# Performance work log

Measured on AMD Instinct MI355X. Metric: run time of the kernel, lower is better.

The kernel has to match this reference:

```python
import jax, jax.numpy as jnp
import numpy as np
from jax import lax


def _conv(x, w, b, stride, pad):
    y = lax.conv_general_dilated(
        x, w, window_strides=(stride, stride),
        padding=[(pad, pad), (pad, pad)],
        dimension_numbers=('NCHW', 'OIHW', 'NCHW'))
    return y + b[None, :, None, None]


def _maxpool3s2(x):
    return lax.reduce_window(x, -jnp.inf, lax.max,
                             (1, 1, 3, 3), (1, 1, 2, 2), 'VALID')


def setup_inputs() -> dict:
    key = jax.random.key(0)
    ks = jax.random.split(key, 16)
    s = 0.05  # weight scale for numerical sanity
    inp = {
        'x': jax.random.normal(ks[0], (128, 3, 224, 224), jnp.float32),
        'w1': jax.random.normal(ks[1], (64, 3, 3, 3), jnp.float32) * s,
        'b1': jnp.zeros((64,), jnp.float32),
        'w2': jax.random.normal(ks[2], (192, 64, 5, 5), jnp.float32) * s,
        'b2': jnp.zeros((192,), jnp.float32),
        'w3': jax.random.normal(ks[3], (384, 192, 3, 3), jnp.float32) * s,
        'b3': jnp.zeros((384,), jnp.float32),
        'w4': jax.random.normal(ks[4], (256, 384, 3, 3), jnp.float32) * s,
        'b4': jnp.zeros((256,), jnp.float32),
        'w5': jax.random.normal(ks[5], (256, 256, 3, 3), jnp.float32) * s,
        'b5': jnp.zeros((256,), jnp.float32),
        'fc1_w': jax.random.normal(ks[6], (4096, 9216), jnp.float32) * 0.01,
        'fc1_b': jnp.zeros((4096,), jnp.float32),
        'fc2_w': jax.random.normal(ks[7], (4096, 4096), jnp.float32) * 0.01,
        'fc2_b': jnp.zeros((4096,), jnp.float32),
        'fc3_w': jax.random.normal(ks[8], (10, 4096), jnp.float32) * 0.01,
        'fc3_b': jnp.zeros((10,), jnp.float32),
        # uniform(0.1, 0.3) per element, matching random.uniform(0.1, 0.3)
        'unif': jax.random.uniform(ks[9], (128, 10), jnp.float32, 0.1, 0.3),
        # np.random.normal(0, 1) noise
        'noise': jax.random.normal(ks[10], (128, 10), jnp.float32),
    }
    return inp


def _forward(x, w1, b1, w2, b2, w3, b3, w4, b4, w5, b5,
             fc1_w, fc1_b, fc2_w, fc2_b, fc3_w, fc3_b, unif, noise):
    # features
    h = jax.nn.relu(_conv(x, w1, b1, stride=4, pad=2))   # [B,64,57,57]
    h = _maxpool3s2(h)                                   # [B,64,28,28]
    h = jax.nn.relu(_conv(h, w2, b2, stride=1, pad=2))   # [B,192,28,28]
    h = _maxpool3s2(h)                                   # [B,192,13,13]
    h = jax.nn.relu(_conv(h, w3, b3, stride=1, pad=1))   # [B,384,13,13]
    h = jax.nn.relu(_conv(h, w4, b4, stride=1, pad=1))   # [B,256,13,13]
    h = jax.nn.relu(_conv(h, w5, b5, stride=1, pad=1))   # [B,256,13,13]
    h = _maxpool3s2(h)                                   # [B,256,6,6]
    # adaptive avgpool to (6,6) is identity at this spatial size
    h = h.reshape(h.shape[0], 256 * 6 * 6)               # [B,9216]
    # classifier (Dropout = identity in eval mode)
    h = jax.nn.relu(h @ fc1_w.T + fc1_b)                 # [B,4096]
    h = jax.nn.relu(h @ fc2_w.T + fc2_b)                 # [B,4096]
    logits = h @ fc3_w.T + fc3_b                         # [B,10]
    # post: keep argmax entry, replace others with unif*max (detached),
    # add Gaussian noise, softmax
    m = jnp.max(logits, axis=-1, keepdims=True)          # [B,1]
    idx = jnp.argmax(logits, axis=-1, keepdims=True)     # first max, like torch
    onehot = jnp.arange(logits.shape[-1])[None, :] == idx
    filled = jnp.where(onehot, logits, unif * lax.stop_gradient(m))
    return jax.nn.softmax(filled + noise, axis=-1)


def reference(x, w1, b1, w2, b2, w3, b3, w4, b4, w5, b5,
              fc1_w, fc1_b, fc2_w, fc2_b, fc3_w, fc3_b, unif, noise):
    return _forward(x, w1, b1, w2, b2, w3, b3, w4, b4, w5, b5,
                    fc1_w, fc1_b, fc2_w, fc2_b, fc3_w, fc3_b, unif, noise)
```

## Files before the change

### kernel.cpp

```cpp
#include <hip/hip_runtime.h>
#include <math.h>


typedef __attribute__((ext_vector_type(4))) float  f32x4;
typedef __attribute__((ext_vector_type(8))) short  bf16x8;

#define OFF_C1O      25690112ull
#define OFF_X2H      0ull
#define OFF_X2L      12845056ull
#define OFF_WT2H     25690112ull
#define OFF_WT2L     26304512ull
#define OFF_WT3H     26918912ull
#define OFF_WT3L     28246016ull
#define OFF_WT4H     29573120ull
#define OFF_WT4L     31342592ull
#define OFF_WT5H     33112064ull
#define OFF_WT5L     34291712ull
#define OFF_Y2H      36000000ull
#define OFF_Y2L      74535168ull
#define OFF_X3H      113100000ull
#define OFF_X3L      121406688ull
#define OFF_Y3H      36000000ull
#define OFF_Y3L      52613376ull
#define OFF_Y4H      70000000ull
#define OFF_Y4L      81075584ull
#define OFF_Y5H      93000000ull
#define OFF_Y5L      104075584ull
#define OFF_P3       0ull
#define OFF_FC1      5000000ull
#define OFF_FC2      8000000ull
#define OFF_LOG      11000000ull
#define OFF_PART     40000000ull

__device__ inline void bf16split(float v, unsigned short& h, unsigned short& l) {
  unsigned u = __builtin_bit_cast(unsigned, v);
  unsigned hb = (u + 0x7fffu + ((u >> 16) & 1u)) >> 16;
  h = (unsigned short)hb;
  float hf = __builtin_bit_cast(float, hb << 16);
  float r = v - hf;
  unsigned u2 = __builtin_bit_cast(unsigned, r);
  l = (unsigned short)((u2 + 0x7fffu + ((u2 >> 16) & 1u)) >> 16);
}
__device__ inline void bf16split_fast(float v, unsigned short& h, unsigned short& l) {
  unsigned u = __builtin_bit_cast(unsigned, v);
  h = (unsigned short)(u >> 16);
  float r = v - __builtin_bit_cast(float, u & 0xFFFF0000u);
  unsigned u2 = __builtin_bit_cast(unsigned, r);
  l = (unsigned short)((u2 + 0x7fffu + ((u2 >> 16) & 1u)) >> 16);
}
__device__ inline float bf2f(unsigned short h) {
  return __builtin_bit_cast(float, ((unsigned)h) << 16);
}

__global__ __launch_bounds__(256) void conv1_kernel(
    const float* __restrict__ x, const float* __restrict__ w,
    const float* __restrict__ bias, float* __restrict__ out) {
  const int b = blockIdx.y;
  const int s = blockIdx.x * 256 + threadIdx.x;
  if (s >= 57 * 57) return;
  const int oh = s / 57, ow = s % 57;
  float iv[27];
#pragma unroll
  for (int ci = 0; ci < 3; ++ci)
#pragma unroll
    for (int kh = 0; kh < 3; ++kh)
#pragma unroll
      for (int kw = 0; kw < 3; ++kw) {
        const int ih = oh * 4 - 2 + kh;
        const int iw = ow * 4 - 2 + kw;
        float v = 0.f;
        if (ih >= 0 && ih < 224 && iw >= 0 && iw < 224)
          v = x[(((size_t)b * 3 + ci) * 224 + ih) * 224 + iw];
        iv[ci * 9 + kh * 3 + kw] = v;
      }
  for (int co = 0; co < 64; ++co) {
    float a = bias[co];
#pragma unroll
    for (int p = 0; p < 27; ++p) a = fmaf(w[co * 27 + p], iv[p], a);
    out[((size_t)b * 64 + co) * 3249 + s] = fmaxf(a, 0.f);
  }
}

__global__ __launch_bounds__(256) void pool1cvt_kernel(
    const float* __restrict__ in, unsigned short* __restrict__ xh,
    unsigned short* __restrict__ xl) {
  const int tid = blockIdx.x * 256 + threadIdx.x;
  if (tid >= 128 * 784) return;
  const int b = tid / 784, s = tid % 784;
  const int oh = s / 28, ow = s % 28;
  const float* base = in + (size_t)b * 64 * 3249 + (size_t)(oh * 2) * 57 + ow * 2;
  for (int cg = 0; cg < 16; ++cg) {
    unsigned short h[4], l[4];
#pragma unroll
    for (int j = 0; j < 4; ++j) {
      const float* p = base + (size_t)(cg * 4 + j) * 3249;
      float m = -INFINITY;
#pragma unroll
      for (int kh = 0; kh < 3; ++kh)
#pragma unroll
        for (int kw = 0; kw < 3; ++kw) m = fmaxf(m, p[kh * 57 + kw]);
      bf16split(m, h[j], l[j]);
    }
    const size_t g = ((size_t)b * 784 + s) * 64 + cg * 4;
    *reinterpret_cast<uint2*>(xh + g) =
        make_uint2((unsigned)h[0] | ((unsigned)h[1] << 16),
                   (unsigned)h[2] | ((unsigned)h[3] << 16));
    *reinterpret_cast<uint2*>(xl + g) =
        make_uint2((unsigned)l[0] | ((unsigned)l[1] << 16),
                   (unsigned)l[2] | ((unsigned)l[3] << 16));
  }
}

__global__ void wtrans_hl_kernel(const float* __restrict__ w,
                                 unsigned short* __restrict__ wh,
                                 unsigned short* __restrict__ wl,
                                 int C_in, int P, int C_out) {
  const int ncc = C_in >> 5;
  const int total = C_out * P * C_in;
  for (int e = blockIdx.x * blockDim.x + threadIdx.x; e < total;
       e += gridDim.x * blockDim.x) {
    const int ci_in = e & 31;
    int t1 = e >> 5;
    const int fr = t1 & 15;
    int t2 = t1 >> 4;
    const int cc = t2 % ncc;
    int t3 = t2 / ncc;
    const int p = t3 % P;
    const int ct = t3 / P;
    const int co = ct * 16 + fr;
    const int ci = cc * 32 + ci_in;
    const float v = w[((size_t)co * C_in + ci) * P + p];
    unsigned short h, l;
    bf16split(v, h, l);
    wh[e] = h; wl[e] = l;
  }
}

__global__ __launch_bounds__(256, 2) void conv2_mfma_kernel(
    const unsigned short* __restrict__ xh, const unsigned short* __restrict__ xl,
    const unsigned short* __restrict__ wh, const unsigned short* __restrict__ wl,
    const float* __restrict__ bias,
    unsigned short* __restrict__ yh, unsigned short* __restrict__ yl) {
  __shared__ unsigned short xt_h[352 * 40];
  __shared__ unsigned short xt_l[352 * 40];
  const int t = threadIdx.x;
  const int lane = t & 63, wv = t >> 6;
  const int b = blockIdx.x;
  const int rg = blockIdx.y;
  const int cg = blockIdx.z;
  const int fr = lane & 15, fq = lane >> 4;
  const int k0 = fq * 8;
  const int frag = fr * 32 + k0;

  int bofs[4];
  bool act[4];
#pragma unroll
  for (int ti = 0; ti < 4; ++ti) {
    const int tile = ti * 4 + wv;
    act[ti] = (tile <= 12);
    int n = tile * 16 + fr;
    if (tile > 12 || n > 195) n = 195;
    const int r = n / 28, c = n % 28;
    bofs[ti] = (r * 32 + c) * 40 + k0;
  }

  f32x4 acc[4][4];
#pragma unroll
  for (int i = 0; i < 4; ++i)
#pragma unroll
    for (int j = 0; j < 4; ++j) acc[i][j] = (f32x4){0.f, 0.f, 0.f, 0.f};

  for (int cc = 0; cc < 2; ++cc) {
    __syncthreads();
    for (int e = t; e < 1408; e += 256) {
      const int sp = e >> 2, kg = e & 3;
      const int hr = sp >> 5, hc = sp & 31;
      const int ih = rg * 7 + hr - 2, ic = hc - 2;
      uint4 vh = make_uint4(0, 0, 0, 0), vl = make_uint4(0, 0, 0, 0);
      if (ih >= 0 && ih < 28 && ic >= 0 && ic < 28) {
        const size_t g = ((size_t)b * 784 + ih * 28 + ic) * 64 + cc * 32 + kg * 8;
        vh = *reinterpret_cast<const uint4*>(xh + g);
        vl = *reinterpret_cast<const uint4*>(xl + g);
      }
      *reinterpret_cast<uint4*>(xt_h + sp * 40 + kg * 8) = vh;
      *reinterpret_cast<uint4*>(xt_l + sp * 40 + kg * 8) = vl;
    }
    __syncthreads();
#pragma unroll 5
    for (int p = 0; p < 25; ++p) {
      bf16x8 a_h[4], a_l[4];
#pragma unroll
      for (int cot = 0; cot < 4; ++cot) {
        const size_t wg = ((((size_t)(cg * 4 + cot) * 25 + p) * 2 + cc) << 9) + frag;
        a_h[cot] = __builtin_bit_cast(bf16x8, *reinterpret_cast<const uint4*>(wh + wg));
        a_l[cot] = __builtin_bit_cast(bf16x8, *reinterpret_cast<const uint4*>(wl + wg));
      }
      const int kh = p / 5, kw = p % 5;
      const int poff = (kh * 32 + kw) * 40;
      bf16x8 bh[4], bl[4];
#pragma unroll
      for (int ti = 0; ti < 4; ++ti) {
        if (act[ti]) {
          bh[ti] = __builtin_bit_cast(bf16x8,
              *reinterpret_cast<const uint4*>(xt_h + bofs[ti] + poff));
          bl[ti] = __builtin_bit_cast(bf16x8,
              *reinterpret_cast<const uint4*>(xt_l + bofs[ti] + poff));
        }
      }
#pragma unroll
      for (int ti = 0; ti < 4; ++ti) if (act[ti])
#pragma unroll
        for (int cot = 0; cot < 4; ++cot)
          acc[ti][cot] = __builtin_amdgcn_mfma_f32_16x16x32_bf16(a_h[cot], bh[ti], acc[ti][cot], 0, 0, 0);
#pragma unroll
      for (int ti = 0; ti < 4; ++ti) if (act[ti])
#pragma unroll
        for (int cot = 0; cot < 4; ++cot)
          acc[ti][cot] = __builtin_amdgcn_mfma_f32_16x16x32_bf16(a_h[cot], bl[ti], acc[ti][cot], 0, 0, 0);
#pragma unroll
      for (int ti = 0; ti < 4; ++ti) if (act[ti])
#pragma unroll
        for (int cot = 0; cot < 4; ++cot)
          acc[ti][cot] = __builtin_amdgcn_mfma_f32_16x16x32_bf16(a_l[cot], bh[ti], acc[ti][cot], 0, 0, 0);
    }
  }
#pragma unroll
  for (int cot = 0; cot < 4; ++cot) {
    const int co = cg * 64 + cot * 16 + fq * 4;
    const float4 bi = *reinterpret_cast<const float4*>(bias + co);
    const float bia[4] = {bi.x, bi.y, bi.z, bi.w};
#pragma unroll
    for (int ti = 0; ti < 4; ++ti) {
      const int tile = ti * 4 + wv;
      if (tile > 12) continue;
      const int n = tile * 16 + fr;
      if (n > 195) continue;
      const int oh = rg * 7 + n / 28, ow = n % 28;
      unsigned short h[4], l[4];
#pragma unroll
      for (int r = 0; r < 4; ++r) {
        const float v = fmaxf(acc[ti][cot][r] + bia[r], 0.f);
        bf16split(v, h[r], l[r]);
      }
      const size_t g = ((size_t)b * 784 + oh * 28 + ow) * 192 + co;
      *reinterpret_cast<uint2*>(yh + g) =
          make_uint2((unsigned)h[0] | ((unsigned)h[1] << 16),
                     (unsigned)h[2] | ((unsigned)h[3] << 16));
      *reinterpret_cast<uint2*>(yl + g) =
          make_uint2((unsigned)l[0] | ((unsigned)l[1] << 16),
                     (unsigned)l[2] | ((unsigned)l[3] << 16));
    }
  }
}

__global__ __launch_bounds__(192) void pool2_hl_kernel(
    const unsigned short* __restrict__ yh, const unsigned short* __restrict__ yl,
    unsigned short* __restrict__ xh, unsigned short* __restrict__ xl) {
  const int b = blockIdx.x, oh = blockIdx.y;
  const int c = threadIdx.x;
  for (int ow = 0; ow < 13; ++ow) {
    float m = -INFINITY;
#pragma unroll
    for (int kh = 0; kh < 3; ++kh)
#pragma unroll
      for (int kw = 0; kw < 3; ++kw) {
        const int s = (oh * 2 + kh) * 28 + (ow * 2 + kw);
        const size_t g = ((size_t)b * 784 + s) * 192 + c;
        m = fmaxf(m, bf2f(yh[g]) + bf2f(yl[g]));
      }
    unsigned short h, l;
    bf16split(m, h, l);
    const size_t gd = ((size_t)b * 169 + oh * 13 + ow) * 192 + c;
    xh[gd] = h; xl[gd] = l;
  }
}

__global__ __launch_bounds__(256, 4) void conv13_mfma_kernel(
    const unsigned short* __restrict__ xh, const unsigned short* __restrict__ xl,
    const unsigned short* __restrict__ wh, const unsigned short* __restrict__ wl,
    const float* __restrict__ bias,
    unsigned short* __restrict__ yh, unsigned short* __restrict__ yl,
    int C_in, int C_out) {
  __shared__ unsigned short xt_h[225 * 40];
  __shared__ unsigned short xt_l[225 * 40];
  const int t = threadIdx.x;
  const int lane = t & 63;
  const int wv = t >> 6;
  const int b = blockIdx.x;
  const int co0 = blockIdx.y * 64 + wv * 16;
  const int ctile = blockIdx.y * 4 + wv;
  const int fr = lane & 15;
  const int fq = lane >> 4;
  const int k0 = fq * 8;
  const int frag = fr * 32 + k0;

  int bofs[11];
#pragma unroll
  for (int nt = 0; nt < 11; ++nt) {
    int n = nt * 16 + fr;
    if (n > 168) n = 168;
    const int oh = n / 13, ow = n % 13;
    bofs[nt] = (oh * 15 + ow) * 40 + k0;
  }

  f32x4 acc[11];
#pragma unroll
  for (int nt = 0; nt < 11; ++nt) acc[nt] = (f32x4){0.f, 0.f, 0.f, 0.f};

  const int ncc = C_in >> 5;
  for (int cc = 0; cc < ncc; ++cc) {
    __syncthreads();
    for (int e = t; e < 900; e += 256) {
      const int sp = e >> 2, kg = e & 3;
      const int r = sp / 15, c = sp % 15;
      const int ir = r - 1, ic = c - 1;
      uint4 vh = make_uint4(0, 0, 0, 0), vl = make_uint4(0, 0, 0, 0);
      if (ir >= 0 && ir < 13 && ic >= 0 && ic < 13) {
        const size_t g = ((size_t)b * 169 + ir * 13 + ic) * C_in + cc * 32 + kg * 8;
        vh = *reinterpret_cast<const uint4*>(xh + g);
        vl = *reinterpret_cast<const uint4*>(xl + g);
      }
      *reinterpret_cast<uint4*>(xt_h + sp * 40 + kg * 8) = vh;
      *reinterpret_cast<uint4*>(xt_l + sp * 40 + kg * 8) = vl;
    }
    __syncthreads();
#pragma unroll
    for (int p = 0; p < 9; ++p) {
      const size_t wg = ((((size_t)ctile * 9 + p) * ncc + cc) << 9) + frag;
      const bf16x8 ca_h = __builtin_bit_cast(bf16x8, *reinterpret_cast<const uint4*>(wh + wg));
      const bf16x8 ca_l = __builtin_bit_cast(bf16x8, *reinterpret_cast<const uint4*>(wl + wg));
      const int poff = ((p / 3) * 15 + (p % 3)) * 40;
#pragma unroll
      for (int q = 0; q < 3; ++q) {
        const int nq = (q < 2) ? 4 : 3;
        bf16x8 bh[4], bl[4];
#pragma unroll
        for (int i = 0; i < 4; ++i) {
          if (i < nq) {
            bh[i] = __builtin_bit_cast(bf16x8,
                *reinterpret_cast<const uint4*>(xt_h + bofs[q * 4 + i] + poff));
            bl[i] = __builtin_bit_cast(bf16x8,
                *reinterpret_cast<const uint4*>(xt_l + bofs[q * 4 + i] + poff));
          }
        }
#pragma unroll
        for (int i = 0; i < 4; ++i) if (i < nq)
          acc[q * 4 + i] = __builtin_amdgcn_mfma_f32_16x16x32_bf16(ca_h, bh[i], acc[q * 4 + i], 0, 0, 0);
#pragma unroll
        for (int i = 0; i < 4; ++i) if (i < nq)
          acc[q * 4 + i] = __builtin_amdgcn_mfma_f32_16x16x32_bf16(ca_h, bl[i], acc[q * 4 + i], 0, 0, 0);
#pragma unroll
        for (int i = 0; i < 4; ++i) if (i < nq)
          acc[q * 4 + i] = __builtin_amdgcn_mfma_f32_16x16x32_bf16(ca_l, bh[i], acc[q * 4 + i], 0, 0, 0);
      }
    }
  }
  const int co_w = co0 + fq * 4;
  const float4 bi = *reinterpret_cast<const float4*>(bias + co_w);
  const float bia[4] = {bi.x, bi.y, bi.z, bi.w};
#pragma unroll
  for (int nt = 0; nt < 11; ++nt) {
    const int n = nt * 16 + fr;
    if (n > 168) continue;
    unsigned short h[4], l[4];
#pragma unroll
    for (int r = 0; r < 4; ++r) {
      float v = fmaxf(acc[nt][r] + bia[r], 0.f);
      bf16split(v, h[r], l[r]);
    }
    const size_t g = ((size_t)b * 169 + n) * C_out + co_w;
    *reinterpret_cast<uint2*>(yh + g) =
        make_uint2((unsigned)h[0] | ((unsigned)h[1] << 16),
                   (unsigned)h[2] | ((unsigned)h[3] << 16));
    *reinterpret_cast<uint2*>(yl + g) =
        make_uint2((unsigned)l[0] | ((unsigned)l[1] << 16),
                   (unsigned)l[2] | ((unsigned)l[3] << 16));
  }
}

__global__ __launch_bounds__(256) void pool3_hl_kernel(
    const unsigned short* __restrict__ yh, const unsigned short* __restrict__ yl,
    float* __restrict__ out) {
  const int b = blockIdx.x;
  const int s2 = blockIdx.y;
  const int c = threadIdx.x;
  const int oh = s2 / 6, ow = s2 % 6;
  float m = -INFINITY;
#pragma unroll
  for (int kh = 0; kh < 3; ++kh)
#pragma unroll
    for (int kw = 0; kw < 3; ++kw) {
      const int si = (oh * 2 + kh) * 13 + (ow * 2 + kw);
      const size_t g = ((size_t)b * 169 + si) * 256 + c;
      m = fmaxf(m, bf2f(yh[g]) + bf2f(yl[g]));
    }
  out[((size_t)b * 256 + c) * 36 + s2] = m;
}

__global__ __launch_bounds__(256, 2) void fc_mfma_kernel(
    const float* __restrict__ act, const float* __restrict__ Wm,
    float* __restrict__ part, int K, int kchunk, int Cout) {
  __shared__ unsigned short ah[128 * 40];
  __shared__ unsigned short al[128 * 40];
  const int t = threadIdx.x;
  const int lane = t & 63, wv = t >> 6;
  const int m0 = blockIdx.x * 128 + wv * 32;
  const int kb = blockIdx.y * kchunk;
  const int fr = lane & 15, fq = lane >> 4;

  f32x4 acc[2][8];
#pragma unroll
  for (int i = 0; i < 2; ++i)
#pragma unroll
    for (int j = 0; j < 8; ++j) acc[i][j] = (f32x4){0.f, 0.f, 0.f, 0.f};

  for (int kc = kb; kc < kb + kchunk; kc += 32) {
    __syncthreads();
#pragma unroll
    for (int i = 0; i < 4; ++i) {
      const int u = t + i * 256;
      const int n = u >> 3, j = u & 7;
      const float4 v = *reinterpret_cast<const float4*>(act + (size_t)n * K + kc + j * 4);
      const float vv[4] = {v.x, v.y, v.z, v.w};
      unsigned short h[4], l[4];
#pragma unroll
      for (int q = 0; q < 4; ++q) bf16split_fast(vv[q], h[q], l[q]);
      *reinterpret_cast<uint2*>(ah + n * 40 + j * 4) =
          make_uint2((unsigned)h[0] | ((unsigned)h[1] << 16),
                     (unsigned)h[2] | ((unsigned)h[3] << 16));
      *reinterpret_cast<uint2*>(al + n * 40 + j * 4) =
          make_uint2((unsigned)l[0] | ((unsigned)l[1] << 16),
                     (unsigned)l[2] | ((unsigned)l[3] << 16));
    }
    __syncthreads();
    bf16x8 a_h[2], a_l[2];
#pragma unroll
    for (int mt = 0; mt < 2; ++mt) {
      const float* wp = Wm + (size_t)(m0 + mt * 16 + fr) * K + kc + fq * 8;
      const float4 w0 = *reinterpret_cast<const float4*>(wp);
      const float4 w1 = *reinterpret_cast<const float4*>(wp + 4);
      const float ws[8] = {w0.x, w0.y, w0.z, w0.w, w1.x, w1.y, w1.z, w1.w};
#pragma unroll
      for (int q = 0; q < 8; ++q) {
        unsigned short h, l;
        bf16split_fast(ws[q], h, l);
        a_h[mt][q] = (short)h;
        a_l[mt][q] = (short)l;
      }
    }
#pragma unroll
    for (int np = 0; np < 4; ++np) {
      bf16x8 bh[2], bl[2];
#pragma unroll
      for (int i = 0; i < 2; ++i) {
        const int nt = np * 2 + i;
        bh[i] = __builtin_bit_cast(bf16x8,
            *reinterpret_cast<const uint4*>(ah + (nt * 16 + fr) * 40 + fq * 8));
        bl[i] = __builtin_bit_cast(bf16x8,
            *reinterpret_cast<const uint4*>(al + (nt * 16 + fr) * 40 + fq * 8));
      }
#pragma unroll
      for (int i = 0; i < 2; ++i)
#pragma unroll
        for (int mt = 0; mt < 2; ++mt)
          acc[mt][np * 2 + i] = __builtin_amdgcn_mfma_f32_16x16x32_bf16(a_h[mt], bh[i], acc[mt][np * 2 + i], 0, 0, 0);
#pragma unroll
      for (int i = 0; i < 2; ++i)
#pragma unroll
        for (int mt = 0; mt < 2; ++mt)
          acc[mt][np * 2 + i] = __builtin_amdgcn_mfma_f32_16x16x32_bf16(a_h[mt], bl[i], acc[mt][np * 2 + i], 0, 0, 0);
#pragma unroll
      for (int i = 0; i < 2; ++i)
#pragma unroll
        for (int mt = 0; mt < 2; ++mt)
          acc[mt][np * 2 + i] = __builtin_amdgcn_mfma_f32_16x16x32_bf16(a_l[mt], bh[i], acc[mt][np * 2 + i], 0, 0, 0);
    }
  }
  const size_t base = (size_t)blockIdx.y * Cout * 128;
#pragma unroll
  for (int mt = 0; mt < 2; ++mt) {
#pragma unroll
    for (int nt = 0; nt < 8; ++nt) {
#pragma unroll
      for (int r = 0; r < 4; ++r) {
        const int m = m0 + mt * 16 + fq * 4 + r;
        const int n = nt * 16 + fr;
        part[base + (size_t)m * 128 + n] = acc[mt][nt][r];
      }
    }
  }
}

__global__ __launch_bounds__(256) void fc_reduce_kernel(
    const float* __restrict__ part, const float* __restrict__ bias,
    float* __restrict__ out, int Cout, int KS, int relu) {
  const int g = blockIdx.x * 256 + threadIdx.x;
  if (g >= Cout * 128) return;
  const int n = g & 127, m = g >> 7;
  float s = 0.f;
  for (int ks = 0; ks < KS; ++ks)
    s += part[(size_t)ks * Cout * 128 + (size_t)m * 128 + n];
  s += bias[m];
  if (relu) s = fmaxf(s, 0.f);
  out[(size_t)n * Cout + m] = s;
}

__global__ __launch_bounds__(256) void fc3_kernel(
    const float* __restrict__ A, const float* __restrict__ W,
    const float* __restrict__ bias, float* __restrict__ out) {
  __shared__ float red[256];
  const int b = blockIdx.x;
  const int t = threadIdx.x;
  float acc[10];
#pragma unroll
  for (int n = 0; n < 10; ++n) acc[n] = 0.f;
  const float* a = A + (size_t)b * 4096;
  for (int k = t; k < 4096; k += 256) {
    const float av = a[k];
#pragma unroll
    for (int n = 0; n < 10; ++n) acc[n] = fmaf(av, W[n * 4096 + k], acc[n]);
  }
  for (int n = 0; n < 10; ++n) {
    red[t] = acc[n];
    __syncthreads();
    for (int off = 128; off > 0; off >>= 1) {
      if (t < off) red[t] += red[t + off];
      __syncthreads();
    }
    if (t == 0) out[b * 10 + n] = red[0] + bias[n];
    __syncthreads();
  }
}

__global__ void post_kernel(const float* __restrict__ logits,
                            const float* __restrict__ unif,
                            const float* __restrict__ noise,
                            float* __restrict__ out) {
  const int b = blockIdx.x * blockDim.x + threadIdx.x;
  if (b >= 128) return;
  float lg[10];
#pragma unroll
  for (int j = 0; j < 10; ++j) lg[j] = logits[b * 10 + j];
  float m = lg[0];
  int idx = 0;
#pragma unroll
  for (int j = 1; j < 10; ++j) {
    if (lg[j] > m) { m = lg[j]; idx = j; }
  }
  float v[10];
#pragma unroll
  for (int j = 0; j < 10; ++j)
    v[j] = ((j == idx) ? lg[j] : unif[b * 10 + j] * m) + noise[b * 10 + j];
  float mx = v[0];
#pragma unroll
  for (int j = 1; j < 10; ++j) mx = fmaxf(mx, v[j]);
  float sum = 0.f;
#pragma unroll
  for (int j = 0; j < 10; ++j) { v[j] = expf(v[j] - mx); sum += v[j]; }
  const float inv = 1.f / sum;
#pragma unroll
  for (int j = 0; j < 10; ++j) out[b * 10 + j] = v[j] * inv;
}

extern "C" void kernel_launch(void* const* d_in, const int* in_sizes, int n_in,
                              void* d_out, int out_size, void* d_ws, size_t ws_size,
                              hipStream_t stream) {
  const float* x     = (const float*)d_in[0];
  const float* w1    = (const float*)d_in[1];
  const float* b1    = (const float*)d_in[2];
  const float* w2    = (const float*)d_in[3];
  const float* b2    = (const float*)d_in[4];
  const float* w3    = (const float*)d_in[5];
  const float* b3    = (const float*)d_in[6];
  const float* w4    = (const float*)d_in[7];
  const float* b4    = (const float*)d_in[8];
  const float* w5    = (const float*)d_in[9];
  const float* b5    = (const float*)d_in[10];
  const float* fc1_w = (const float*)d_in[11];
  const float* fc1_b = (const float*)d_in[12];
  const float* fc2_w = (const float*)d_in[13];
  const float* fc2_b = (const float*)d_in[14];
  const float* fc3_w = (const float*)d_in[15];
  const float* fc3_b = (const float*)d_in[16];
  const float* unif  = (const float*)d_in[17];
  const float* noise = (const float*)d_in[18];
  float* out = (float*)d_out;

  char* W = (char*)d_ws;
#define FP(off) ((float*)(W + (off)))
#define US(off) ((unsigned short*)(W + (off)))

  conv1_kernel<<<dim3(13, 128), 256, 0, stream>>>(x, w1, b1, FP(OFF_C1O));
  pool1cvt_kernel<<<392, 256, 0, stream>>>(FP(OFF_C1O), US(OFF_X2H), US(OFF_X2L));
  wtrans_hl_kernel<<<512, 256, 0, stream>>>(w2, US(OFF_WT2H), US(OFF_WT2L), 64, 25, 192);
  wtrans_hl_kernel<<<512, 256, 0, stream>>>(w3, US(OFF_WT3H), US(OFF_WT3L), 192, 9, 384);
  wtrans_hl_kernel<<<512, 256, 0, stream>>>(w4, US(OFF_WT4H), US(OFF_WT4L), 384, 9, 256);
  wtrans_hl_kernel<<<512, 256, 0, stream>>>(w5, US(OFF_WT5H), US(OFF_WT5L), 256, 9, 256);
  conv2_mfma_kernel<<<dim3(128, 4, 3), 256, 0, stream>>>(
      US(OFF_X2H), US(OFF_X2L), US(OFF_WT2H), US(OFF_WT2L), b2,
      US(OFF_Y2H), US(OFF_Y2L));
  pool2_hl_kernel<<<dim3(128, 13), 192, 0, stream>>>(
      US(OFF_Y2H), US(OFF_Y2L), US(OFF_X3H), US(OFF_X3L));
  conv13_mfma_kernel<<<dim3(128, 6), 256, 0, stream>>>(
      US(OFF_X3H), US(OFF_X3L), US(OFF_WT3H), US(OFF_WT3L), b3,
      US(OFF_Y3H), US(OFF_Y3L), 192, 384);
  conv13_mfma_kernel<<<dim3(128, 4), 256, 0, stream>>>(
      US(OFF_Y3H), US(OFF_Y3L), US(OFF_WT4H), US(OFF_WT4L), b4,
      US(OFF_Y4H), US(OFF_Y4L), 384, 256);
  conv13_mfma_kernel<<<dim3(128, 4), 256, 0, stream>>>(
      US(OFF_Y4H), US(OFF_Y4L), US(OFF_WT5H), US(OFF_WT5L), b5,
      US(OFF_Y5H), US(OFF_Y5L), 256, 256);
  pool3_hl_kernel<<<dim3(128, 36), 256, 0, stream>>>(US(OFF_Y5H), US(OFF_Y5L), FP(OFF_P3));
  fc_mfma_kernel<<<dim3(32, 16), 256, 0, stream>>>(FP(OFF_P3), fc1_w, FP(OFF_PART), 9216, 576, 4096);
  fc_reduce_kernel<<<2048, 256, 0, stream>>>(FP(OFF_PART), fc1_b, FP(OFF_FC1), 4096, 16, 1);
  fc_mfma_kernel<<<dim3(32, 16), 256, 0, stream>>>(FP(OFF_FC1), fc2_w, FP(OFF_PART), 4096, 256, 4096);
  fc_reduce_kernel<<<2048, 256, 0, stream>>>(FP(OFF_PART), fc2_b, FP(OFF_FC2), 4096, 16, 1);
  fc3_kernel<<<128, 256, 0, stream>>>(FP(OFF_FC2), fc3_w, fc3_b, FP(OFF_LOG));
  post_kernel<<<1, 128, 0, stream>>>(FP(OFF_LOG), unif, noise, out);
}
```

Baseline: 740.0 us.

## Split conv2 hi/lo input passes to halve shared memory and raise occupancy

The conv2 MFMA kernel now stages only one bf16 half of the input tile in shared memory at a time. It runs the hi×hi and lo×hi products in a first pass, then reloads the tile with the lo half and runs hi×lo in a second pass. This halves LDS usage and the per-iteration B-fragment registers, and the launch bound goes from 2 to 4 blocks per CU to allow higher occupancy. In exchange it adds an extra tile load with two more barriers per channel chunk, and reloads the hi weights in the second pass.

```diff
diff --git a/kernel.cpp b/kernel.cpp
--- a/kernel.cpp
+++ b/kernel.cpp
@@ -136,13 +136,12 @@
   }
 }
 
-__global__ __launch_bounds__(256, 2) void conv2_mfma_kernel(
+__global__ __launch_bounds__(256, 4) void conv2_mfma_kernel(
     const unsigned short* __restrict__ xh, const unsigned short* __restrict__ xl,
     const unsigned short* __restrict__ wh, const unsigned short* __restrict__ wl,
     const float* __restrict__ bias,
     unsigned short* __restrict__ yh, unsigned short* __restrict__ yl) {
-  __shared__ unsigned short xt_h[352 * 40];
-  __shared__ unsigned short xt_l[352 * 40];
+  __shared__ unsigned short xt[352 * 40];
   const int t = threadIdx.x;
   const int lane = t & 63, wv = t >> 6;
   const int b = blockIdx.x;
@@ -176,14 +175,11 @@
       const int sp = e >> 2, kg = e & 3;
       const int hr = sp >> 5, hc = sp & 31;
       const int ih = rg * 7 + hr - 2, ic = hc - 2;
-      uint4 vh = make_uint4(0, 0, 0, 0), vl = make_uint4(0, 0, 0, 0);
-      if (ih >= 0 && ih < 28 && ic >= 0 && ic < 28) {
-        const size_t g = ((size_t)b * 784 + ih * 28 + ic) * 64 + cc * 32 + kg * 8;
-        vh = *reinterpret_cast<const uint4*>(xh + g);
-        vl = *reinterpret_cast<const uint4*>(xl + g);
-      }
-      *reinterpret_cast<uint4*>(xt_h + sp * 40 + kg * 8) = vh;
-      *reinterpret_cast<uint4*>(xt_l + sp * 40 + kg * 8) = vl;
+      uint4 v = make_uint4(0, 0, 0, 0);
+      if (ih >= 0 && ih < 28 && ic >= 0 && ic < 28)
+        v = *reinterpret_cast<const uint4*>(
+            xh + ((size_t)b * 784 + ih * 28 + ic) * 64 + cc * 32 + kg * 8);
+      *reinterpret_cast<uint4*>(xt + sp * 40 + kg * 8) = v;
     }
     __syncthreads();
 #pragma unroll 5
@@ -197,16 +193,12 @@
       }
       const int kh = p / 5, kw = p % 5;
       const int poff = (kh * 32 + kw) * 40;
-      bf16x8 bh[4], bl[4];
-#pragma unroll
-      for (int ti = 0; ti < 4; ++ti) {
-        if (act[ti]) {
+      bf16x8 bh[4];
+#pragma unroll
+      for (int ti = 0; ti < 4; ++ti)
+        if (act[ti])
           bh[ti] = __builtin_bit_cast(bf16x8,
-              *reinterpret_cast<const uint4*>(xt_h + bofs[ti] + poff));
-          bl[ti] = __builtin_bit_cast(bf16x8,
-              *reinterpret_cast<const uint4*>(xt_l + bofs[ti] + poff));
-        }
-      }
+              *reinterpret_cast<const uint4*>(xt + bofs[ti] + poff));
 #pragma unroll
       for (int ti = 0; ti < 4; ++ti) if (act[ti])
 #pragma unroll
@@ -216,12 +208,41 @@
       for (int ti = 0; ti < 4; ++ti) if (act[ti])
 #pragma unroll
         for (int cot = 0; cot < 4; ++cot)
+          acc[ti][cot] = __builtin_amdgcn_mfma_f32_16x16x32_bf16(a_l[cot], bh[ti], acc[ti][cot], 0, 0, 0);
+    }
+    __syncthreads();
+    for (int e = t; e < 1408; e += 256) {
+      const int sp = e >> 2, kg = e & 3;
+      const int hr = sp >> 5, hc = sp & 31;
+      const int ih = rg * 7 + hr - 2, ic = hc - 2;
+      uint4 v = make_uint4(0, 0, 0, 0);
+      if (ih >= 0 && ih < 28 && ic >= 0 && ic < 28)
+        v = *reinterpret_cast<const uint4*>(
+            xl + ((size_t)b * 784 + ih * 28 + ic) * 64 + cc * 32 + kg * 8);
+      *reinterpret_cast<uint4*>(xt + sp * 40 + kg * 8) = v;
+    }
+    __syncthreads();
+#pragma unroll 5
+    for (int p = 0; p < 25; ++p) {
+      bf16x8 a_h[4];
+#pragma unroll
+      for (int cot = 0; cot < 4; ++cot) {
+        const size_t wg = ((((size_t)(cg * 4 + cot) * 25 + p) * 2 + cc) << 9) + frag;
+        a_h[cot] = __builtin_bit_cast(bf16x8, *reinterpret_cast<const uint4*>(wh + wg));
+      }
+      const int kh = p / 5, kw = p % 5;
+      const int poff = (kh * 32 + kw) * 40;
+      bf16x8 bl[4];
+#pragma unroll
+      for (int ti = 0; ti < 4; ++ti)
+        if (act[ti])
+          bl[ti] = __builtin_bit_cast(bf16x8,
+              *reinterpret_cast<const uint4*>(xt + bofs[ti] + poff));
+#pragma unroll
+      for (int ti = 0; ti < 4; ++ti) if (act[ti])
+#pragma unroll
+        for (int cot = 0; cot < 4; ++cot)
           acc[ti][cot] = __builtin_amdgcn_mfma_f32_16x16x32_bf16(a_h[cot], bl[ti], acc[ti][cot], 0, 0, 0);
-#pragma unroll
-      for (int ti = 0; ti < 4; ++ti) if (act[ti])
-#pragma unroll
-        for (int cot = 0; cot < 4; ++cot)
-          acc[ti][cot] = __builtin_amdgcn_mfma_f32_16x16x32_bf16(a_l[cot], bh[ti], acc[ti][cot], 0, 0, 0);
     }
   }
 #pragma unroll
```

Result: slower. 1.548 ms (+109.2%).
